# Kernel optimization log

Hardware: AMD Instinct MI355X
Metric: run time of the kernel (lower is better)

Reference implementation:

```python
import jax, jax.numpy as jnp
import numpy as np

HIDDEN = 2048
NUM_HEADS = 32
NUM_KV_HEADS = 8
HEAD_DIM = 128
EPS = 1e-6
ROPE_BASE = 10000.0
T = 2048


def setup_inputs() -> dict:
    key = jax.random.key(0)
    k1, k2, k3, k4, k5 = jax.random.split(key, 5)
    q_size = NUM_HEADS * HEAD_DIM
    kv_size = NUM_KV_HEADS * HEAD_DIM
    s = 0.02
    return {
        "positions": jnp.arange(T, dtype=jnp.int32),
        "hidden_states": jax.random.normal(k1, (T, HIDDEN), dtype=jnp.float32),
        "wqkv": jax.random.normal(k2, (q_size + 2 * kv_size, HIDDEN), dtype=jnp.float32) * s,
        "wo": jax.random.normal(k3, (HIDDEN, q_size), dtype=jnp.float32) * s,
        "q_norm_w": jnp.ones((HEAD_DIM,), dtype=jnp.float32),
        "k_norm_w": jnp.ones((HEAD_DIM,), dtype=jnp.float32),
    }


def _rms_norm(x, w, eps=EPS):
    # x: [T, H, D]; normalize over last dim
    var = jnp.mean(jnp.square(x), axis=-1, keepdims=True)
    return x * jax.lax.rsqrt(var + eps) * w


def _rope(positions, x):
    # neox-style rotate-half RoPE. x: [T, H, D]
    half = HEAD_DIM // 2
    inv_freq = 1.0 / (ROPE_BASE ** (jnp.arange(0, half, dtype=jnp.float32) / half))
    ang = positions.astype(jnp.float32)[:, None] * inv_freq  # [T, half]
    cos = jnp.cos(ang)[:, None, :]  # [T, 1, half]
    sin = jnp.sin(ang)[:, None, :]
    x1, x2 = x[..., :half], x[..., half:]
    return jnp.concatenate([x1 * cos - x2 * sin, x2 * cos + x1 * sin], axis=-1)


def reference(positions, hidden_states, wqkv, wo, q_norm_w, k_norm_w):
    q_size = NUM_HEADS * HEAD_DIM
    kv_size = NUM_KV_HEADS * HEAD_DIM
    scaling = HEAD_DIM ** -0.5

    qkv = hidden_states @ wqkv.T  # [T, q_size + 2*kv_size]
    q = qkv[:, :q_size].reshape(-1, NUM_HEADS, HEAD_DIM)
    k = qkv[:, q_size:q_size + kv_size].reshape(-1, NUM_KV_HEADS, HEAD_DIM)
    v = qkv[:, q_size + kv_size:].reshape(-1, NUM_KV_HEADS, HEAD_DIM)

    q = _rms_norm(q, q_norm_w)
    k = _rms_norm(k, k_norm_w)
    q = _rope(positions, q)
    k = _rope(positions, k)

    # GQA: repeat kv heads to match query heads
    group = NUM_HEADS // NUM_KV_HEADS
    k = jnp.repeat(k, group, axis=1)  # [T, H, D]
    v = jnp.repeat(v, group, axis=1)

    scores = jnp.einsum("thd,shd->hts", q, k) * scaling  # [H, T, T]
    causal = positions[:, None] >= positions[None, :]  # [T, T]
    scores = jnp.where(causal[None], scores, jnp.finfo(scores.dtype).min)
    probs = jax.nn.softmax(scores, axis=-1)
    o = jnp.einsum("hts,shd->thd", probs, v)  # [T, H, D]
    return o.reshape(-1, q_size) @ wo.T  # [T, HIDDEN]
```

## Files before the change

### kernel.cpp

```cpp
#include <hip/hip_runtime.h>
#include <hip/hip_bf16.h>

#define T_SEQ   2048
#define HIDDEN  2048
#define NUM_H   32
#define NUM_KV  8
#define HD      128
#define Q_SIZE  4096
#define QKV_N   6144

typedef __bf16 bf16;
typedef __bf16 bf16x8 __attribute__((ext_vector_type(8)));
typedef __bf16 bf16x4 __attribute__((ext_vector_type(4)));
typedef float  floatx4 __attribute__((ext_vector_type(4)));

#define GLOBAL_AS(p) ((const __attribute__((address_space(1))) void*)(p))
#define LDS_AS(p)    ((__attribute__((address_space(3))) void*)(p))

#define BARRIER() do { asm volatile("" ::: "memory"); \
                       __builtin_amdgcn_s_barrier();  \
                       asm volatile("" ::: "memory"); } while (0)
#define VMCNT(n) asm volatile("s_waitcnt vmcnt(" #n ")" ::: "memory")
#define SCHED()  __builtin_amdgcn_sched_barrier(0)

__device__ __forceinline__ int detect_bf16(const unsigned short* __restrict__ wq)
{
    const int lane = threadIdx.x & 63;
    int cnt = 0;
    for (int i = lane; i < 512; i += 64) {
        int ef = (wq[i] >> 7) & 0xFF;
        if (ef >= 90 && ef <= 130) cnt++;
    }
    #pragma unroll
    for (int m = 32; m; m >>= 1) cnt += __shfl_xor(cnt, m);
    return (cnt >= 430) ? 1 : 0;
}

__global__ __launch_bounds__(256) void convert_all(
    const void* __restrict__ h, const void* __restrict__ wq,
    const void* __restrict__ wo_, const void* __restrict__ qn,
    const void* __restrict__ kn,
    bf16* __restrict__ hb, bf16* __restrict__ wqb, bf16* __restrict__ wob,
    bf16* __restrict__ qnb, bf16* __restrict__ knb)
{
    const int flag = detect_bf16((const unsigned short*)wq);

    long e = ((long)blockIdx.x * 256 + threadIdx.x) * 8;
    const void* src; bf16* dst; long off;
    if      (e < 4194304)  { src = h;   dst = hb;  off = e; }
    else if (e < 16777216) { src = wq;  dst = wqb; off = e - 4194304; }
    else if (e < 25165824) { src = wo_; dst = wob; off = e - 16777216; }
    else if (e < 25165952) { src = qn;  dst = qnb; off = e - 25165824; }
    else if (e < 25166080) { src = kn;  dst = knb; off = e - 25165952; }
    else return;

    if (flag) {
        *(bf16x8*)(dst + off) = *(const bf16x8*)((const bf16*)src + off);
    } else {
        const float* f = (const float*)src + off;
        bf16x8 v;
        #pragma unroll
        for (int i = 0; i < 8; ++i) v[i] = (bf16)f[i];
        *(bf16x8*)(dst + off) = v;
    }
}

__global__ __launch_bounds__(512, 2) void gemm3p(
    const bf16* __restrict__ A, const bf16* __restrict__ B,
    bf16* __restrict__ C, int N, int K, int lda, int ldb)
{
    __shared__ bf16 As[2][2][128 * 64];
    __shared__ bf16 Bs[2][192 * 64];

    const int tid  = threadIdx.x;
    const int wave = tid >> 6, lane = tid & 63;
    const int quad = lane >> 4, l16 = lane & 15;
    const int wm = wave >> 2;
    const int wn = wave & 3;
    const long baseN = (long)blockIdx.x * 192;
    const long baseM = (long)blockIdx.y * 256;

    const int sr  = tid >> 3;
    const int sgc = ((tid & 7) ^ (sr & 7)) * 8;

    auto stagePA = [&](int p, int g, int t) {
        const long kc = (long)t * 64;
        const bf16* src = A + (baseM + g * 64 + sr) * (long)lda + kc + sgc;
        __builtin_amdgcn_global_load_lds(GLOBAL_AS(src),
            LDS_AS(&As[p][0][g * 4096 + wave * 512]), 16, 0, 0);
        __builtin_amdgcn_global_load_lds(GLOBAL_AS(src + 128 * (long)lda),
            LDS_AS(&As[p][1][g * 4096 + wave * 512]), 16, 0, 0);
    };
    auto stagePBu = [&](int p, int u, int t) {
        const long kc = (long)t * 64;
        const bf16* src = B + (baseN + u * 64 + sr) * (long)ldb + kc + sgc;
        __builtin_amdgcn_global_load_lds(GLOBAL_AS(src),
            LDS_AS(&Bs[p][u * 4096 + wave * 512]), 16, 0, 0);
    };

    floatx4 acc[8][3] = {};
    bf16x8 af0[4][2], af1[4][2], bf01[2][2], bf2[2];

    auto rdAf0 = [&](int p) {
        #pragma unroll
        for (int mf = 0; mf < 4; ++mf)
            #pragma unroll
            for (int ks = 0; ks < 2; ++ks) {
                const int r = mf * 16 + l16;
                af0[mf][ks] = *(const bf16x8*)(&As[p][wm][r * 64 + (((ks * 4 + quad) ^ (r & 7)) * 8)]);
            }
    };
    auto rdAf1 = [&](int p) {
        #pragma unroll
        for (int mf = 0; mf < 4; ++mf)
            #pragma unroll
            for (int ks = 0; ks < 2; ++ks) {
                const int r = 64 + mf * 16 + l16;
                af1[mf][ks] = *(const bf16x8*)(&As[p][wm][r * 64 + (((ks * 4 + quad) ^ (r & 7)) * 8)]);
            }
    };
    auto rdB01 = [&](int p) {
        #pragma unroll
        for (int nf = 0; nf < 2; ++nf)
            #pragma unroll
            for (int ks = 0; ks < 2; ++ks) {
                const int r = wn * 48 + nf * 16 + l16;
                bf01[nf][ks] = *(const bf16x8*)(&Bs[p][r * 64 + (((ks * 4 + quad) ^ (r & 7)) * 8)]);
            }
    };
    auto rdB2 = [&](int p) {
        #pragma unroll
        for (int ks = 0; ks < 2; ++ks) {
            const int r = wn * 48 + 32 + l16;
            bf2[ks] = *(const bf16x8*)(&Bs[p][r * 64 + (((ks * 4 + quad) ^ (r & 7)) * 8)]);
        }
    };

    auto mmA0B01 = [&]() {
        __builtin_amdgcn_s_setprio(1);
        #pragma unroll
        for (int mf = 0; mf < 4; ++mf)
            #pragma unroll
            for (int nf = 0; nf < 2; ++nf)
                #pragma unroll
                for (int ks = 0; ks < 2; ++ks)
                    acc[mf][nf] = __builtin_amdgcn_mfma_f32_16x16x32_bf16(
                        af0[mf][ks], bf01[nf][ks], acc[mf][nf], 0, 0, 0);
        __builtin_amdgcn_s_setprio(0);
    };
    auto mmB2 = [&]() {
        __builtin_amdgcn_s_setprio(1);
        #pragma unroll
        for (int mf = 0; mf < 4; ++mf)
            #pragma unroll
            for (int ks = 0; ks < 2; ++ks)
                acc[mf][2] = __builtin_amdgcn_mfma_f32_16x16x32_bf16(
                    af0[mf][ks], bf2[ks], acc[mf][2], 0, 0, 0);
        #pragma unroll
        for (int mf = 0; mf < 4; ++mf)
            #pragma unroll
            for (int ks = 0; ks < 2; ++ks)
                acc[4 + mf][2] = __builtin_amdgcn_mfma_f32_16x16x32_bf16(
                    af1[mf][ks], bf2[ks], acc[4 + mf][2], 0, 0, 0);
        __builtin_amdgcn_s_setprio(0);
    };
    auto mmA1B01 = [&]() {
        __builtin_amdgcn_s_setprio(1);
        #pragma unroll
        for (int mf = 0; mf < 4; ++mf)
            #pragma unroll
            for (int nf = 0; nf < 2; ++nf)
                #pragma unroll
                for (int ks = 0; ks < 2; ++ks)
                    acc[4 + mf][nf] = __builtin_amdgcn_mfma_f32_16x16x32_bf16(
                        af1[mf][ks], bf01[nf][ks], acc[4 + mf][nf], 0, 0, 0);
        __builtin_amdgcn_s_setprio(0);
    };

    stagePBu(0, 0, 0); stagePBu(0, 1, 0); stagePBu(0, 2, 0);
    stagePA(0, 0, 0);  stagePA(0, 1, 0);
    VMCNT(2);
    BARRIER();

    const int NT = K / 64;
    for (int t = 0; t < NT; ++t) {
        const int p = t & 1;
        const bool more = (t + 1 < NT);

        rdAf0(p); rdB01(p); rdB2(p);
        if (more) {
            stagePBu(p ^ 1, 0, t + 1); stagePBu(p ^ 1, 1, t + 1); stagePBu(p ^ 1, 2, t + 1);
            VMCNT(3);
        } else {
            VMCNT(0);
        }
        BARRIER(); SCHED();
        mmA0B01();
        BARRIER();

        rdAf1(p);
        if (more) stagePA(p ^ 1, 0, t + 1);
        BARRIER(); SCHED();
        mmB2();
        BARRIER();

        if (more) { stagePA(p ^ 1, 1, t + 1); VMCNT(2); }
        SCHED();
        mmA1B01();
        BARRIER();
    }

    #pragma unroll
    for (int i = 0; i < 8; ++i)
        #pragma unroll
        for (int j = 0; j < 3; ++j)
            #pragma unroll
            for (int r = 0; r < 4; ++r) {
                long row = baseM + wm * 128 + i * 16 + quad * 4 + r;
                long col = baseN + wn * 48 + j * 16 + l16;
                C[row * (long)N + col] = (bf16)acc[i][j][r];
            }
}

__global__ __launch_bounds__(256, 2) void gemm_db64(
    const bf16* __restrict__ A, const bf16* __restrict__ B,
    float* __restrict__ Cp, int N, int Kd, int lda, int ldb)
{
    __shared__ bf16 As[2][128 * 64];
    __shared__ bf16 Bs[2][128 * 64];

    const int tid  = threadIdx.x;
    const int wave = tid >> 6, lane = tid & 63;
    const int quad = lane >> 4, l16 = lane & 15;
    const int wm = (wave & 1) * 64, wn = (wave >> 1) * 64;
    const long baseM = (long)blockIdx.x * 128;
    const long baseN = (long)blockIdx.y * 128;
    const long koff  = (long)blockIdx.z * Kd;

    const int sr  = tid >> 3;
    const int sgc = ((tid & 7) ^ (sr & 7)) * 8;

    auto stage = [&](int p, int t) {
        const long kc = koff + (long)t * 64;
        #pragma unroll
        for (int u = 0; u < 4; ++u) {
            const bf16* sa = A + (baseM + u * 32 + sr) * (long)lda + kc + sgc;
            __builtin_amdgcn_global_load_lds(GLOBAL_AS(sa),
                LDS_AS(&As[p][u * 2048 + wave * 512]), 16, 0, 0);
        }
        #pragma unroll
        for (int u = 0; u < 4; ++u) {
            const bf16* sb = B + (baseN + u * 32 + sr) * (long)ldb + kc + sgc;
            __builtin_amdgcn_global_load_lds(GLOBAL_AS(sb),
                LDS_AS(&Bs[p][u * 2048 + wave * 512]), 16, 0, 0);
        }
    };

    floatx4 acc[4][4] = {};

    stage(0, 0);

    const int NT = Kd / 64;
    int cur = 0;
    for (int t = 0; t < NT; ++t) {
        if (t + 1 < NT) { stage(cur ^ 1, t + 1); VMCNT(8); }
        else            { VMCNT(0); }
        BARRIER();

        bf16x8 af[4][2], bfr[4][2];
        #pragma unroll
        for (int i = 0; i < 4; ++i)
            #pragma unroll
            for (int ks = 0; ks < 2; ++ks) {
                const int r = wm + i * 16 + l16;
                af[i][ks] = *(const bf16x8*)(&As[cur][r * 64 + (((ks * 4 + quad) ^ (r & 7)) * 8)]);
            }
        #pragma unroll
        for (int j = 0; j < 4; ++j)
            #pragma unroll
            for (int ks = 0; ks < 2; ++ks) {
                const int r = wn + j * 16 + l16;
                bfr[j][ks] = *(const bf16x8*)(&Bs[cur][r * 64 + (((ks * 4 + quad) ^ (r & 7)) * 8)]);
            }

        __builtin_amdgcn_s_setprio(1);
        #pragma unroll
        for (int i = 0; i < 4; ++i)
            #pragma unroll
            for (int j = 0; j < 4; ++j)
                #pragma unroll
                for (int ks = 0; ks < 2; ++ks)
                    acc[i][j] = __builtin_amdgcn_mfma_f32_16x16x32_bf16(
                        af[i][ks], bfr[j][ks], acc[i][j], 0, 0, 0);
        __builtin_amdgcn_s_setprio(0);

        BARRIER();
        cur ^= 1;
    }

    const long Mrows = (long)gridDim.x * 128;
    float* C = Cp + (long)blockIdx.z * Mrows * N;
    #pragma unroll
    for (int i = 0; i < 4; ++i)
        #pragma unroll
        for (int j = 0; j < 4; ++j)
            #pragma unroll
            for (int r = 0; r < 4; ++r) {
                long row = baseM + wm + i * 16 + quad * 4 + r;
                long col = baseN + wn + j * 16 + l16;
                C[row * (long)N + col] = acc[i][j][r];
            }
}

__global__ __launch_bounds__(256) void reduce2(
    const float* __restrict__ P0, const float* __restrict__ P1,
    void* __restrict__ out, const unsigned short* __restrict__ wq)
{
    const int flag = detect_bf16(wq);

    long i = ((long)blockIdx.x * 256 + threadIdx.x) * 4;
    floatx4 a = *(const floatx4*)(P0 + i);
    floatx4 b = *(const floatx4*)(P1 + i);
    floatx4 s = a + b;
    if (flag) {
        bf16x4 o;
        #pragma unroll
        for (int r = 0; r < 4; ++r) o[r] = (bf16)s[r];
        *(bf16x4*)((bf16*)out + i) = o;
    } else {
        *(floatx4*)((float*)out + i) = s;
    }
}

__global__ __launch_bounds__(256) void post_fused(
    bf16* __restrict__ qkv, const int* __restrict__ positions,
    const bf16* __restrict__ qnw, const bf16* __restrict__ knw,
    bf16* __restrict__ vt)
{
    __shared__ bf16 tile[64][136];
    const int bid = blockIdx.x, tid = threadIdx.x;

    if (bid < T_SEQ) {
        const int t = bid, wave = tid >> 6, lane = tid & 63;
        const float pos = (float)positions[t];

        const float inv = expf(-(float)lane * (float)(9.210340371976184 / 64.0));
        float sn, cs;
        sincosf(pos * inv, &sn, &cs);

        bf16* row = qkv + (long)t * QKV_N;

        for (int u = wave; u < 40; u += 4) {
            bf16* p       = (u < 32) ? row + u * HD : row + Q_SIZE + (u - 32) * HD;
            const bf16* w = (u < 32) ? qnw : knw;
            float x1 = (float)p[lane], x2 = (float)p[lane + 64];
            float ss = x1 * x1 + x2 * x2;
            #pragma unroll
            for (int m = 32; m; m >>= 1) ss += __shfl_xor(ss, m);
            float rr = rsqrtf(ss * (1.f / 128.f) + 1e-6f);
            float y1 = x1 * rr * (float)w[lane];
            float y2 = x2 * rr * (float)w[lane + 64];
            p[lane]      = (bf16)(y1 * cs - y2 * sn);
            p[lane + 64] = (bf16)(y2 * cs + y1 * sn);
        }
    } else {
        const int vb = bid - T_SEQ;
        const int t0 = (vb & 31) * 64, kvh = vb >> 5;

        const int rl = tid >> 4, c8 = (tid & 15) * 8;
        const bf16* src = qkv + (long)t0 * QKV_N + 5120 + kvh * HD;
        #pragma unroll
        for (int it = 0; it < 4; ++it) {
            int r = it * 16 + rl;
            *(bf16x8*)(&tile[r][c8]) = *(const bf16x8*)(src + (long)r * QKV_N + c8);
        }
        __syncthreads();

        const int d = tid >> 1, tb = (tid & 1) * 32;
        bf16* dst = vt + ((long)kvh * HD + d) * T_SEQ + t0 + tb;
        #pragma unroll
        for (int it = 0; it < 4; ++it) {
            bf16x8 v;
            #pragma unroll
            for (int j = 0; j < 8; ++j) v[j] = tile[tb + it * 8 + j][d];
            *(bf16x8*)(dst + it * 8) = v;
        }
    }
}

__global__ __launch_bounds__(256, 3) void attn5(bf16* qkv, const bf16* __restrict__ vt)
{
    __shared__ bf16 Ks[2][64 * 128];
    __shared__ bf16 Vs[128 * 64];

    const int tid  = threadIdx.x, wave = tid >> 6, lane = tid & 63;
    const int quad = lane >> 4, l16 = lane & 15;
    const int h = blockIdx.x, kvh = h >> 2;
    const int iq = 31 - blockIdx.y;
    const int q0 = iq * 64;

    const float C1 = 0.12753236f;
    const float C2 = 17.312340f;

    bf16x8 qf[4];
    {
        const bf16* qa = qkv + (long)(q0 + wave * 16 + l16) * QKV_N + h * HD + quad * 8;
        #pragma unroll
        for (int ks = 0; ks < 4; ++ks) qf[ks] = *(const bf16x8*)(qa + ks * 32);
    }

    floatx4 oacc[8] = {};
    float ls = 0.f;

    const int krl = lane >> 4, kc = lane & 15;
    const int vrl = lane >> 3, vc = lane & 7;
    const int kswz = (kc ^ (wave * 4 + krl)) * 8;
    const int vswz = (vc ^ (vrl & 7)) * 8;
    const int wsig = ((wave & 1) << 1) | (wave >> 1);
    const int sq4  = (((quad & 1) << 1) | (quad >> 1)) << 2;

    const bf16* kg0 = qkv + Q_SIZE + kvh * HD;
    const bf16* vg0 = vt + (long)kvh * HD * T_SEQ;

    auto stageK = [&](int p, int kt) {
        const bf16* kg = kg0 + (long)(kt * 64) * QKV_N;
        #pragma unroll
        for (int it = 0; it < 4; ++it) {
            const int rK = it * 16 + wsig * 4 + krl;
            __builtin_amdgcn_global_load_lds(GLOBAL_AS(kg + (long)rK * QKV_N + kswz),
                                             LDS_AS(&Ks[p][it * 2048 + wave * 512]), 16, 0, 0);
        }
    };
    auto stageV = [&](int kt) {
        const bf16* vg = vg0 + kt * 64;
        #pragma unroll
        for (int it = 0; it < 4; ++it) {
            const int dV = it * 32 + wave * 8 + vrl;
            __builtin_amdgcn_global_load_lds(GLOBAL_AS(vg + (long)dV * T_SEQ + vswz),
                                             LDS_AS(&Vs[it * 2048 + wave * 512]), 16, 0, 0);
        }
    };

    stageK(0, 0);

    const int qg = q0 + wave * 16 + l16;

    for (int kt = 0; kt <= iq; ++kt) {
        const int p = kt & 1;
        __syncthreads();
        stageV(kt);
        if (kt < iq) stageK(p ^ 1, kt + 1);

        const int k0 = kt * 64;

        floatx4 sT[4] = {};
        #pragma unroll
        for (int j2 = 0; j2 < 4; ++j2)
            #pragma unroll
            for (int ks = 0; ks < 4; ++ks) {
                bf16x8 kf = *(const bf16x8*)(&Ks[p][(j2 * 16 + l16) * 128 + (((ks * 4 + quad) ^ l16) * 8)]);
                sT[j2] = __builtin_amdgcn_mfma_f32_16x16x32_bf16(kf, qf[ks], sT[j2], 0, 0, 0);
            }

        const bool diag = (kt == iq);
        unsigned lov[4], hiv[4];
        #pragma unroll
        for (int j2 = 0; j2 < 4; ++j2) {
            float ev[4];
            #pragma unroll
            for (int r = 0; r < 4; ++r) {
                float x = __builtin_amdgcn_exp2f(sT[j2][r] * C1 - C2);
                if (diag && (k0 + j2 * 16 + sq4 + r > qg)) x = 0.f;
                ls += x;
                ev[r] = x;
            }
            asm("v_cvt_pk_bf16_f32 %0, %1, %2" : "=v"(lov[j2]) : "v"(ev[0]), "v"(ev[1]));
            asm("v_cvt_pk_bf16_f32 %0, %1, %2" : "=v"(hiv[j2]) : "v"(ev[2]), "v"(ev[3]));
        }

        bf16x8 pa[2];
        #pragma unroll
        for (int ks2 = 0; ks2 < 2; ++ks2) {
            auto wl = __builtin_amdgcn_permlane32_swap(lov[2 * ks2], lov[2 * ks2 + 1], false, false);
            auto wh = __builtin_amdgcn_permlane32_swap(hiv[2 * ks2], hiv[2 * ks2 + 1], false, false);
            union { unsigned w[4]; bf16x8 v; } u;
            u.w[0] = wl[0]; u.w[1] = wh[0]; u.w[2] = wl[1]; u.w[3] = wh[1];
            pa[ks2] = u.v;
        }

        if (kt < iq) asm volatile("s_waitcnt vmcnt(4)" ::: "memory");
        else         asm volatile("s_waitcnt vmcnt(0)" ::: "memory");
        __builtin_amdgcn_s_barrier();
        __builtin_amdgcn_sched_barrier(0);

        #pragma unroll
        for (int ks2 = 0; ks2 < 2; ++ks2)
            #pragma unroll
            for (int vj = 0; vj < 8; ++vj) {
                const int d = vj * 16 + l16;
                bf16x8 vb = *(const bf16x8*)(&Vs[d * 64 + (((ks2 * 4 + quad) ^ (d & 7)) * 8)]);
                oacc[vj] = __builtin_amdgcn_mfma_f32_16x16x32_bf16(pa[ks2], vb, oacc[vj], 0, 0, 0);
            }
    }

    ls += __shfl_xor(ls, 16); ls += __shfl_xor(ls, 32);
    float rinv[4];
    #pragma unroll
    for (int r = 0; r < 4; ++r) rinv[r] = 1.f / __shfl(ls, quad * 4 + r);

    #pragma unroll
    for (int vj = 0; vj < 8; ++vj)
        #pragma unroll
        for (int r = 0; r < 4; ++r) {
            const long row = q0 + wave * 16 + quad * 4 + r;
            qkv[row * (long)QKV_N + h * HD + vj * 16 + l16] = (bf16)(oacc[vj][r] * rinv[r]);
        }
}

extern "C" void kernel_launch(void* const* d_in, const int* in_sizes, int n_in,
                              void* d_out, int out_size, void* d_ws, size_t ws_size,
                              hipStream_t stream)
{
    const int* positions = (const int*)d_in[0];

    char* ws = (char*)d_ws;
    bf16* qkv  = (bf16*)(ws);
    bf16* hb   = (bf16*)(ws + 25165824);
    bf16* vt   = hb;
    float* P0  = (float*)(ws + 25165824);
    float* P1  = (float*)(ws + 41943040);
    bf16* wqb  = (bf16*)(ws + 33554432);
    bf16* wob  = (bf16*)(ws + 58720256);
    bf16* qnb  = (bf16*)(ws + 75497472);
    bf16* knb  = (bf16*)(ws + 75497728);

    convert_all<<<dim3(12289), dim3(256), 0, stream>>>(
        d_in[1], d_in[2], d_in[3], d_in[4], d_in[5],
        hb, wqb, wob, qnb, knb);

    gemm3p<<<dim3(QKV_N / 192, T_SEQ / 256), dim3(512), 0, stream>>>(
        hb, wqb, qkv, QKV_N, HIDDEN, HIDDEN, HIDDEN);
    post_fused<<<dim3(T_SEQ + 256), dim3(256), 0, stream>>>(
        qkv, positions, qnb, knb, vt);
    attn5<<<dim3(NUM_H, 32), dim3(256), 0, stream>>>(qkv, vt);
    gemm_db64<<<dim3(T_SEQ / 128, HIDDEN / 128, 2), dim3(256), 0, stream>>>(
        qkv, wob, P0, HIDDEN, Q_SIZE / 2, QKV_N, Q_SIZE);
    reduce2<<<dim3(4096), dim3(256), 0, stream>>>(
        P0, P1, d_out, (const unsigned short*)d_in[2]);
}
```

Baseline: 308.9 us.

## Restructure output projection GEMM into 256x128 tiles with split-phase A/B prefetch

Replaces the 128x128, 256-thread output-projection GEMM with a 512-thread kernel computing 256x128 tiles. The K loop is split into two phases per step, each staging part of the next tile (B first, then A) while MFMAs run on the current half, which gives finer-grained overlap. The grid is also reordered so blockIdx.x walks N. Larger tiles cut redundant global loads of the weight matrix, but LDS use grows (96KB per block) and extra barriers are added, which may lower occupancy.

```diff
diff --git a/kernel.cpp b/kernel.cpp
--- a/kernel.cpp
+++ b/kernel.cpp
@@ -222,92 +222,124 @@
             }
 }
 
-__global__ __launch_bounds__(256, 2) void gemm_db64(
+__global__ __launch_bounds__(512, 2) void gemm_o2p(
     const bf16* __restrict__ A, const bf16* __restrict__ B,
     float* __restrict__ Cp, int N, int Kd, int lda, int ldb)
 {
-    __shared__ bf16 As[2][128 * 64];
+    __shared__ bf16 As[2][2][128 * 64];
     __shared__ bf16 Bs[2][128 * 64];
 
     const int tid  = threadIdx.x;
     const int wave = tid >> 6, lane = tid & 63;
     const int quad = lane >> 4, l16 = lane & 15;
-    const int wm = (wave & 1) * 64, wn = (wave >> 1) * 64;
-    const long baseM = (long)blockIdx.x * 128;
-    const long baseN = (long)blockIdx.y * 128;
+    const int wm = wave >> 2;
+    const int wn = wave & 3;
+    const long baseN = (long)blockIdx.x * 128;
+    const long baseM = (long)blockIdx.y * 256;
     const long koff  = (long)blockIdx.z * Kd;
 
     const int sr  = tid >> 3;
     const int sgc = ((tid & 7) ^ (sr & 7)) * 8;
 
-    auto stage = [&](int p, int t) {
+    auto stagePA = [&](int p, int g, int t) {
         const long kc = koff + (long)t * 64;
-        #pragma unroll
-        for (int u = 0; u < 4; ++u) {
-            const bf16* sa = A + (baseM + u * 32 + sr) * (long)lda + kc + sgc;
-            __builtin_amdgcn_global_load_lds(GLOBAL_AS(sa),
-                LDS_AS(&As[p][u * 2048 + wave * 512]), 16, 0, 0);
-        }
-        #pragma unroll
-        for (int u = 0; u < 4; ++u) {
-            const bf16* sb = B + (baseN + u * 32 + sr) * (long)ldb + kc + sgc;
-            __builtin_amdgcn_global_load_lds(GLOBAL_AS(sb),
-                LDS_AS(&Bs[p][u * 2048 + wave * 512]), 16, 0, 0);
-        }
-    };
-
-    floatx4 acc[4][4] = {};
-
-    stage(0, 0);
-
-    const int NT = Kd / 64;
-    int cur = 0;
-    for (int t = 0; t < NT; ++t) {
-        if (t + 1 < NT) { stage(cur ^ 1, t + 1); VMCNT(8); }
-        else            { VMCNT(0); }
-        BARRIER();
-
-        bf16x8 af[4][2], bfr[4][2];
-        #pragma unroll
-        for (int i = 0; i < 4; ++i)
+        const bf16* src = A + (baseM + g * 64 + sr) * (long)lda + kc + sgc;
+        __builtin_amdgcn_global_load_lds(GLOBAL_AS(src),
+            LDS_AS(&As[p][0][g * 4096 + wave * 512]), 16, 0, 0);
+        __builtin_amdgcn_global_load_lds(GLOBAL_AS(src + 128 * (long)lda),
+            LDS_AS(&As[p][1][g * 4096 + wave * 512]), 16, 0, 0);
+    };
+    auto stagePBu = [&](int p, int u, int t) {
+        const long kc = koff + (long)t * 64;
+        const bf16* src = B + (baseN + u * 64 + sr) * (long)ldb + kc + sgc;
+        __builtin_amdgcn_global_load_lds(GLOBAL_AS(src),
+            LDS_AS(&Bs[p][u * 4096 + wave * 512]), 16, 0, 0);
+    };
+
+    floatx4 acc[8][2] = {};
+    bf16x8 af0[4][2], af1[4][2], bfr[2][2];
+
+    auto rdAf0 = [&](int p) {
+        #pragma unroll
+        for (int mf = 0; mf < 4; ++mf)
             #pragma unroll
             for (int ks = 0; ks < 2; ++ks) {
-                const int r = wm + i * 16 + l16;
-                af[i][ks] = *(const bf16x8*)(&As[cur][r * 64 + (((ks * 4 + quad) ^ (r & 7)) * 8)]);
-            }
-        #pragma unroll
-        for (int j = 0; j < 4; ++j)
+                const int r = mf * 16 + l16;
+                af0[mf][ks] = *(const bf16x8*)(&As[p][wm][r * 64 + (((ks * 4 + quad) ^ (r & 7)) * 8)]);
+            }
+    };
+    auto rdAf1 = [&](int p) {
+        #pragma unroll
+        for (int mf = 0; mf < 4; ++mf)
             #pragma unroll
             for (int ks = 0; ks < 2; ++ks) {
-                const int r = wn + j * 16 + l16;
-                bfr[j][ks] = *(const bf16x8*)(&Bs[cur][r * 64 + (((ks * 4 + quad) ^ (r & 7)) * 8)]);
-            }
-
+                const int r = 64 + mf * 16 + l16;
+                af1[mf][ks] = *(const bf16x8*)(&As[p][wm][r * 64 + (((ks * 4 + quad) ^ (r & 7)) * 8)]);
+            }
+    };
+    auto rdB = [&](int p) {
+        #pragma unroll
+        for (int nf = 0; nf < 2; ++nf)
+            #pragma unroll
+            for (int ks = 0; ks < 2; ++ks) {
+                const int r = wn * 32 + nf * 16 + l16;
+                bfr[nf][ks] = *(const bf16x8*)(&Bs[p][r * 64 + (((ks * 4 + quad) ^ (r & 7)) * 8)]);
+            }
+    };
+    auto mm16 = [&](bf16x8 (&af)[4][2], int mo) {
         __builtin_amdgcn_s_setprio(1);
         #pragma unroll
-        for (int i = 0; i < 4; ++i)
-            #pragma unroll
-            for (int j = 0; j < 4; ++j)
+        for (int mf = 0; mf < 4; ++mf)
+            #pragma unroll
+            for (int nf = 0; nf < 2; ++nf)
                 #pragma unroll
                 for (int ks = 0; ks < 2; ++ks)
-                    acc[i][j] = __builtin_amdgcn_mfma_f32_16x16x32_bf16(
-                        af[i][ks], bfr[j][ks], acc[i][j], 0, 0, 0);
+                    acc[mo + mf][nf] = __builtin_amdgcn_mfma_f32_16x16x32_bf16(
+                        af[mf][ks], bfr[nf][ks], acc[mo + mf][nf], 0, 0, 0);
         __builtin_amdgcn_s_setprio(0);
-
+    };
+
+    stagePBu(0, 0, 0); stagePBu(0, 1, 0);
+    stagePA(0, 0, 0);  stagePA(0, 1, 0);
+    VMCNT(2);
+    BARRIER();
+
+    const int NT = Kd / 64;
+    for (int t = 0; t < NT; ++t) {
+        const int p = t & 1;
+        const bool more = (t + 1 < NT);
+
+        rdAf0(p); rdB(p);
+        if (more) {
+            stagePBu(p ^ 1, 0, t + 1); stagePBu(p ^ 1, 1, t + 1);
+            VMCNT(2);
+        } else {
+            VMCNT(0);
+        }
+        BARRIER(); SCHED();
+        mm16(af0, 0);
         BARRIER();
-        cur ^= 1;
-    }
-
-    const long Mrows = (long)gridDim.x * 128;
+
+        rdAf1(p);
+        if (more) {
+            stagePA(p ^ 1, 0, t + 1); stagePA(p ^ 1, 1, t + 1);
+            VMCNT(2);
+        }
+        BARRIER(); SCHED();
+        mm16(af1, 4);
+        BARRIER();
+    }
+
+    const long Mrows = (long)gridDim.y * 256;
     float* C = Cp + (long)blockIdx.z * Mrows * N;
     #pragma unroll
-    for (int i = 0; i < 4; ++i)
-        #pragma unroll
-        for (int j = 0; j < 4; ++j)
+    for (int i = 0; i < 8; ++i)
+        #pragma unroll
+        for (int j = 0; j < 2; ++j)
             #pragma unroll
             for (int r = 0; r < 4; ++r) {
-                long row = baseM + wm + i * 16 + quad * 4 + r;
-                long col = baseN + wn + j * 16 + l16;
+                long row = baseM + wm * 128 + i * 16 + quad * 4 + r;
+                long col = baseN + wn * 32 + j * 16 + l16;
                 C[row * (long)N + col] = acc[i][j][r];
             }
 }
@@ -543,7 +575,7 @@
     post_fused<<<dim3(T_SEQ + 256), dim3(256), 0, stream>>>(
         qkv, positions, qnb, knb, vt);
     attn5<<<dim3(NUM_H, 32), dim3(256), 0, stream>>>(qkv, vt);
-    gemm_db64<<<dim3(T_SEQ / 128, HIDDEN / 128, 2), dim3(256), 0, stream>>>(
+    gemm_o2p<<<dim3(HIDDEN / 128, T_SEQ / 256, 2), dim3(512), 0, stream>>>(
         qkv, wob, P0, HIDDEN, Q_SIZE / 2, QKV_N, Q_SIZE);
     reduce2<<<dim3(4096), dim3(256), 0, stream>>>(
         P0, P1, d_out, (const unsigned short*)d_in[2]);
```

New measurement: 314.5 us. Within noise of the previous version (+1.8%).
